# Performance work log

Measured on AMD Instinct MI355X. Metric: run time of the kernel, lower is better.

## Reference

```python
import jax, jax.numpy as jnp
import numpy as np

BLOCKS = 8
SSM_SIZE = 512
D_MODEL = 1024
DT_MIN = 1e-3
DT_MAX = 0.1
STEP_RESCALE = 1.0
BATCH = 4
SEQ_LEN = 4096


def _make_dplr_hippo(N):
    # numpy double-precision HiPPO-LegS -> DPLR init (done once at setup)
    n = np.arange(N, dtype=np.float64)
    P = np.sqrt(1.0 + 2.0 * n)
    A = -(np.tril(P[:, None] * P[None, :]) - np.diag(n))
    Pv = np.sqrt(n + 0.5)
    S = A + Pv[:, None] * Pv[None, :]
    Lambda_real = np.mean(np.diag(S)) + np.ones(N)
    Lambda_imag, V = np.linalg.eigh(S * -1j)  # V: (N, N) complex
    return Lambda_real + 1j * Lambda_imag, V


def _block_diag(M, reps):
    N = M.shape[0]
    out = np.zeros((N * reps, N * reps), dtype=M.dtype)
    for i in range(reps):
        out[i * N:(i + 1) * N, i * N:(i + 1) * N] = M
    return out


def setup_inputs() -> dict:
    key = jax.random.key(0)
    k1, k2, k3, k4, k5 = jax.random.split(key, 5)
    bs = SSM_SIZE // BLOCKS
    Lam_blk, V_blk = _make_dplr_hippo(bs)
    Lambda = np.tile(Lam_blk, BLOCKS)                     # (ssm_size,)
    V = _block_diag(V_blk, BLOCKS)                        # (ssm_size, ssm_size)
    Vinv = _block_diag(V_blk.conj().T, BLOCKS)

    Vc = jnp.asarray(V, dtype=jnp.complex64)
    Vinvc = jnp.asarray(Vinv, dtype=jnp.complex64)

    B0 = jax.random.normal(k1, (SSM_SIZE, D_MODEL), dtype=jnp.float32)
    VinvB = Vinvc @ B0.astype(jnp.complex64)              # (ssm_size, d_model)
    B = jnp.stack([VinvB.real, VinvB.imag], axis=-1)      # (ssm_size, d_model, 2)

    C0 = jax.random.normal(k2, (D_MODEL, SSM_SIZE, 2), dtype=jnp.float32)
    CV = (C0[..., 0] + 1j * C0[..., 1]).astype(jnp.complex64) @ Vc
    C = jnp.stack([CV.real, CV.imag], axis=-1)            # (d_model, ssm_size, 2)

    D = jax.random.normal(k3, (D_MODEL,), dtype=jnp.float32)
    step = jnp.log(jax.random.uniform(k4, (SSM_SIZE, 1)) * (DT_MAX - DT_MIN) + DT_MIN)

    u = jax.random.normal(k5, (BATCH, SEQ_LEN, D_MODEL), dtype=jnp.float32)
    return {
        "u": u,
        "Lambda_re": jnp.asarray(Lambda.real, dtype=jnp.float32),
        "Lambda_imag": jnp.asarray(Lambda.imag, dtype=jnp.float32),
        "B": B,
        "C": C,
        "D": D,
        "step": step,
    }


def _scan_binop(e1, e2):
    a1, b1 = e1
    a2, b2 = e2
    return a1 * a2, a2 * b1 + b2


def reference(u, Lambda_re, Lambda_imag, B, C, D, step):
    # clip_eigs=True
    Lambda = jnp.minimum(Lambda_re, -1e-4) + 1j * Lambda_imag      # (N,) complex
    B_tilde = B[..., 0] + 1j * B[..., 1]                           # (N, H)
    C_tilde = C[..., 0] + 1j * C[..., 1]                           # (H, N)
    dt = STEP_RESCALE * jnp.exp(step.squeeze(-1))                  # (N,)
    # ZOH discretization
    Lambda_bar = jnp.exp(Lambda * dt)                              # (N,)
    B_bar = ((Lambda_bar - 1.0) / Lambda)[:, None] * B_tilde       # (N, H)
    # input projection into state space
    Bu = u.astype(jnp.complex64) @ B_bar.T                         # (B, L, N)
    # linear recurrence x_t = Lambda_bar * x_{t-1} + Bu_t via associative scan
    A = jnp.broadcast_to(Lambda_bar, Bu.shape)
    _, state = jax.lax.associative_scan(_scan_binop, (A, Bu), axis=1)  # (B, L, N)
    y = (state @ C_tilde.T).real + D * u                           # (B, L, H)
    y = jax.nn.relu(y)
    return y, state
```

## Files before the change

### kernel.cpp

```cpp
#include <hip/hip_runtime.h>
#include <hip/hip_bf16.h>

typedef __attribute__((ext_vector_type(8))) short short8;
typedef __attribute__((ext_vector_type(4))) float f32x4;

#define DEVI __device__ __forceinline__

constexpr int SEQ = 4096;
constexpr int HD = 1024;
constexpr int NS = 512;
constexpr int NB = 4;
constexpr int MROWS = NB * SEQ;
constexpr int NCH = 64;
constexpr int CLEN = SEQ / NCH;

constexpr size_t MB = 1024 * 1024;
constexpr size_t OFF_UBF = 0;
constexpr size_t OFF_W1  = 32 * MB;
constexpr size_t OFF_W2  = 34 * MB;
constexpr size_t OFF_P   = 36 * MB;
constexpr size_t OFF_BU  = 36 * MB + 65536;
constexpr size_t OFF_T   = OFF_BU + 32 * MB;
constexpr size_t OFF_CRY = OFF_T + 1 * MB;
constexpr size_t OFF_SBF = OFF_CRY + 1 * MB;
constexpr size_t OFF_STF = OFF_SBF + 32 * MB;

DEVI float bf2f(unsigned short u) {
    union { unsigned u32; float f; } x; x.u32 = (unsigned)u << 16; return x.f;
}

__global__ void prep_params(const float* __restrict__ Lre, const float* __restrict__ Lim,
                            const float* __restrict__ step, float* __restrict__ P) {
    int n = blockIdx.x * 64 + threadIdx.x;
    if (n >= NS) return;
    float dt  = expf(step[n]);
    float lre = fminf(Lre[n], -1e-4f);
    float lim = Lim[n];
    float wre = lre * dt, wim = lim * dt;
    float s, c;
    sincosf(wim, &s, &c);
    float e = expf(wre);
    float lbre = e * c, lbim = e * s;
    float em1 = expm1f(wre);
    float sh  = sinf(0.5f * wim);
    float nr  = em1 * c - 2.0f * sh * sh;
    float ni  = e * s;
    float d2  = lre * lre + lim * lim;
    float inv = 1.0f / d2;
    float fre = (nr * lre + ni * lim) * inv;
    float fim = (ni * lre - nr * lim) * inv;
    float* p = P + n * 6;
    p[0] = wre; p[1] = wim; p[2] = lbre; p[3] = lbim; p[4] = fre; p[5] = fim;
}

__global__ void build_weights(const float* __restrict__ Bin, const float* __restrict__ Cin,
                              const float* __restrict__ P,
                              __hip_bfloat16* __restrict__ W1t,
                              __hip_bfloat16* __restrict__ W2t) {
    int bid = blockIdx.x;
    if (bid < 2048) {
        int idx = bid * 256 + threadIdx.x;
        int n = idx >> 10, k = idx & 1023;
        float fre = P[n * 6 + 4], fim = P[n * 6 + 5];
        float bre = Bin[(size_t)idx * 2 + 0], bim = Bin[(size_t)idx * 2 + 1];
        W1t[(size_t)(2 * n) * HD + k]     = __float2bfloat16(fre * bre - fim * bim);
        W1t[(size_t)(2 * n + 1) * HD + k] = __float2bfloat16(fre * bim + fim * bre);
    } else {
        int idx = (bid - 2048) * 256 + threadIdx.x;
        int h = idx >> 9, n = idx & 511;
        float cre = Cin[(size_t)idx * 2 + 0], cim = Cin[(size_t)idx * 2 + 1];
        W2t[(size_t)h * HD + 2 * n]     = __float2bfloat16(cre);
        W2t[(size_t)h * HD + 2 * n + 1] = __float2bfloat16(-cim);
    }
}

__global__ void cast_to_bf16(const float* __restrict__ x, __hip_bfloat16* __restrict__ y, int n8) {
    int i = blockIdx.x * 256 + threadIdx.x;
    if (i >= n8) return;
    const float4* xv = (const float4*)x;
    float4 a = xv[2 * (size_t)i], b = xv[2 * (size_t)i + 1];
    union { __hip_bfloat16 h[8]; short8 v; } u8;
    u8.h[0] = __float2bfloat16(a.x); u8.h[1] = __float2bfloat16(a.y);
    u8.h[2] = __float2bfloat16(a.z); u8.h[3] = __float2bfloat16(a.w);
    u8.h[4] = __float2bfloat16(b.x); u8.h[5] = __float2bfloat16(b.y);
    u8.h[6] = __float2bfloat16(b.z); u8.h[7] = __float2bfloat16(b.w);
    *((short8*)(y + (size_t)i * 8)) = u8.v;
}

DEVI void gload16(const __hip_bfloat16* g, __hip_bfloat16* l) {
    __builtin_amdgcn_global_load_lds(
        (const __attribute__((address_space(1))) unsigned int*)g,
        (__attribute__((address_space(3))) unsigned int*)l,
        16, 0, 0);
}

#define BARRIER_RAW() { asm volatile("" ::: "memory"); __builtin_amdgcn_s_barrier(); asm volatile("" ::: "memory"); }

template <int EPI>
__global__ __launch_bounds__(512, 2) void gemm_bf16_256(
    const __hip_bfloat16* __restrict__ A,
    const __hip_bfloat16* __restrict__ Bt,
    void* __restrict__ CoutV,
    const float* __restrict__ Dvec,
    const __hip_bfloat16* __restrict__ Ubf)
{
    __shared__ __hip_bfloat16 As[2][256 * 64];
    __shared__ __hip_bfloat16 Bs[2][256 * 64];
    const int tid  = threadIdx.x;
    const int lane = tid & 63;
    const int wid  = tid >> 6;
    const size_t bm = (size_t)blockIdx.x * 256;
    const size_t bn = (size_t)blockIdx.y * 256;
    const int wr = (wid >> 2) * 128;
    const int wc = (wid & 3) * 64;
    const int fr = lane & 15;
    const int fq = lane >> 4;

    f32x4 acc[8][4];
#pragma unroll
    for (int i = 0; i < 8; ++i)
#pragma unroll
        for (int j = 0; j < 4; ++j) acc[i][j] = (f32x4){0.f, 0.f, 0.f, 0.f};

    const int srow = tid >> 3;
    const int schk = tid & 7;

#define STAGE(buf, kt)                                                          \
    {                                                                           \
        _Pragma("unroll")                                                       \
        for (int q = 0; q < 4; ++q) {                                           \
            int row = q * 64 + srow;                                            \
            int gcol = (schk ^ (row & 7)) * 8;                                  \
            gload16(A  + (bm + row) * 1024 + (kt) + gcol, &As[buf][(row * 8 + schk) * 8]); \
            gload16(Bt + (bn + row) * 1024 + (kt) + gcol, &Bs[buf][(row * 8 + schk) * 8]); \
        }                                                                       \
    }

    STAGE(0, 0);
    __syncthreads();

    int cur = 0;
    for (int t = 0; t < 16; ++t) {
        if (t < 15) {
            STAGE(cur ^ 1, (t + 1) * 64);
            asm volatile("s_waitcnt vmcnt(8)" ::: "memory");
        } else {
            asm volatile("s_waitcnt vmcnt(0)" ::: "memory");
        }
        __builtin_amdgcn_sched_barrier(0);
        BARRIER_RAW();

#pragma unroll
        for (int kh = 0; kh < 2; ++kh) {
            short8 af[8], bf_[4];
#pragma unroll
            for (int m = 0; m < 8; ++m) {
                int r = wr + m * 16 + fr;
                int pc = (kh * 4 + fq) ^ (r & 7);
                af[m] = *(const short8*)(&As[cur][(r * 8 + pc) * 8]);
            }
#pragma unroll
            for (int n = 0; n < 4; ++n) {
                int r = wc + n * 16 + fr;
                int pc = (kh * 4 + fq) ^ (r & 7);
                bf_[n] = *(const short8*)(&Bs[cur][(r * 8 + pc) * 8]);
            }
#pragma unroll
            for (int m = 0; m < 8; ++m)
#pragma unroll
                for (int n = 0; n < 4; ++n)
                    acc[m][n] = __builtin_amdgcn_mfma_f32_16x16x32_bf16(af[m], bf_[n], acc[m][n], 0, 0, 0);
        }
        BARRIER_RAW();
        cur ^= 1;
    }
#undef STAGE

#pragma unroll
    for (int m = 0; m < 8; ++m)
#pragma unroll
        for (int n = 0; n < 4; ++n) {
            size_t col = bn + wc + n * 16 + fr;
            float dcol = (EPI == 1) ? Dvec[col] : 0.0f;
#pragma unroll
            for (int r = 0; r < 4; ++r) {
                size_t row = bm + wr + m * 16 + fq * 4 + r;
                float v = acc[m][n][r];
                if (EPI == 1) {
                    v = fmaf(dcol, __bfloat162float(Ubf[row * 1024 + col]), v);
                    ((float*)CoutV)[row * 1024 + col] = fmaxf(v, 0.0f);
                } else {
                    ((__hip_bfloat16*)CoutV)[row * 1024 + col] = __float2bfloat16(v);
                }
            }
        }
}

__global__ __launch_bounds__(256) void scan_totals(const unsigned* __restrict__ Bub,
                                                   const float* __restrict__ P,
                                                   float* __restrict__ T) {
    const int b = blockIdx.x >> 6;
    const int c = blockIdx.x & 63;
    const int t = threadIdx.x;
    const float l0r = P[t * 6 + 2], l0i = P[t * 6 + 3];
    const float l1r = P[(t + 256) * 6 + 2], l1i = P[(t + 256) * 6 + 3];
    const unsigned* base = Bub + ((size_t)(b * SEQ + c * CLEN)) * 512;
    float x0r = 0.f, x0i = 0.f, x1r = 0.f, x1i = 0.f;
    for (int j = 0; j < CLEN; ++j) {
        unsigned p0 = base[(size_t)j * 512 + t];
        unsigned p1 = base[(size_t)j * 512 + t + 256];
        float v0x = bf2f((unsigned short)(p0 & 0xffff)), v0y = bf2f((unsigned short)(p0 >> 16));
        float v1x = bf2f((unsigned short)(p1 & 0xffff)), v1y = bf2f((unsigned short)(p1 >> 16));
        float nr = fmaf(l0r, x0r, fmaf(-l0i, x0i, v0x));
        float ni = fmaf(l0r, x0i, fmaf(l0i, x0r, v0y));
        x0r = nr; x0i = ni;
        nr = fmaf(l1r, x1r, fmaf(-l1i, x1i, v1x));
        ni = fmaf(l1r, x1i, fmaf(l1i, x1r, v1y));
        x1r = nr; x1i = ni;
    }
    float2* Tp = (float2*)T;
    size_t o = ((size_t)(b * NCH + c)) * 512;
    Tp[o + t]       = make_float2(x0r, x0i);
    Tp[o + t + 256] = make_float2(x1r, x1i);
}

__global__ __launch_bounds__(256) void scan_carry(const float* __restrict__ T,
                                                  const float* __restrict__ P,
                                                  float* __restrict__ Cry) {
    int idx = blockIdx.x * 256 + threadIdx.x;
    if (idx >= NB * NS) return;
    int b = idx >> 9, n = idx & 511;
    float wre = P[n * 6 + 0] * (float)CLEN, wim = P[n * 6 + 1] * (float)CLEN;
    float s, c;
    sincosf(wim, &s, &c);
    float e = expf(wre);
    float cr = e * c, ci = e * s;
    float xr = 0.f, xi = 0.f;
    const float2* Tp = (const float2*)T;
    float2* Cp = (float2*)Cry;
    for (int ch = 0; ch < NCH; ++ch) {
        size_t o = ((size_t)(b * NCH + ch)) * 512 + n;
        Cp[o] = make_float2(xr, xi);
        float2 tv = Tp[o];
        float nr = fmaf(cr, xr, fmaf(-ci, xi, tv.x));
        float ni = fmaf(cr, xi, fmaf(ci, xr, tv.y));
        xr = nr; xi = ni;
    }
}

__global__ __launch_bounds__(256) void scan_final(const unsigned* __restrict__ Bub,
                                                  const float* __restrict__ P,
                                                  const float* __restrict__ Cry,
                                                  float* __restrict__ Sre,
                                                  __hip_bfloat16* __restrict__ Sbf) {
    const int b = blockIdx.x >> 6;
    const int c = blockIdx.x & 63;
    const int t = threadIdx.x;
    const float l0r = P[t * 6 + 2], l0i = P[t * 6 + 3];
    const float l1r = P[(t + 256) * 6 + 2], l1i = P[(t + 256) * 6 + 3];
    const unsigned* base = Bub + ((size_t)(b * SEQ + c * CLEN)) * 512;
    const float2* Cp = (const float2*)Cry;
    size_t co = ((size_t)(b * NCH + c)) * 512;
    float2 c0 = Cp[co + t], c1 = Cp[co + t + 256];
    float x0r = c0.x, x0i = c0.y, x1r = c1.x, x1i = c1.y;
    for (int j = 0; j < CLEN; ++j) {
        unsigned p0 = base[(size_t)j * 512 + t];
        unsigned p1 = base[(size_t)j * 512 + t + 256];
        float v0x = bf2f((unsigned short)(p0 & 0xffff)), v0y = bf2f((unsigned short)(p0 >> 16));
        float v1x = bf2f((unsigned short)(p1 & 0xffff)), v1y = bf2f((unsigned short)(p1 >> 16));
        float nr = fmaf(l0r, x0r, fmaf(-l0i, x0i, v0x));
        float ni = fmaf(l0r, x0i, fmaf(l0i, x0r, v0y));
        x0r = nr; x0i = ni;
        nr = fmaf(l1r, x1r, fmaf(-l1i, x1i, v1x));
        ni = fmaf(l1r, x1i, fmaf(l1i, x1r, v1y));
        x1r = nr; x1i = ni;
        size_t m = (size_t)b * SEQ + c * CLEN + j;
        Sre[m * 512 + t]       = x0r;
        Sre[m * 512 + t + 256] = x1r;
        union { __hip_bfloat16 h[2]; unsigned uu; } q0, q1;
        q0.h[0] = __float2bfloat16(x0r); q0.h[1] = __float2bfloat16(x0i);
        q1.h[0] = __float2bfloat16(x1r); q1.h[1] = __float2bfloat16(x1i);
        *((unsigned*)(Sbf + m * 1024 + 2 * t))       = q0.uu;
        *((unsigned*)(Sbf + m * 1024 + 2 * t + 512)) = q1.uu;
    }
}

extern "C" void kernel_launch(void* const* d_in, const int* in_sizes, int n_in,
                              void* d_out, int out_size, void* d_ws, size_t ws_size,
                              hipStream_t stream) {
    const float* u    = (const float*)d_in[0];
    const float* Lre  = (const float*)d_in[1];
    const float* Lim  = (const float*)d_in[2];
    const float* Bin  = (const float*)d_in[3];
    const float* Cin  = (const float*)d_in[4];
    const float* Dv   = (const float*)d_in[5];
    const float* step = (const float*)d_in[6];

    char* ws = (char*)d_ws;
    __hip_bfloat16* Ubf = (__hip_bfloat16*)(ws + OFF_UBF);
    __hip_bfloat16* W1t = (__hip_bfloat16*)(ws + OFF_W1);
    __hip_bfloat16* W2t = (__hip_bfloat16*)(ws + OFF_W2);
    float*          P   = (float*)(ws + OFF_P);
    __hip_bfloat16* Bu  = (__hip_bfloat16*)(ws + OFF_BU);
    float*          T   = (float*)(ws + OFF_T);
    float*          Cry = (float*)(ws + OFF_CRY);
    __hip_bfloat16* Sbf = (__hip_bfloat16*)(ws + OFF_SBF);

    float* y_out = (float*)d_out;
    constexpr int Y_ELEMS = MROWS * HD;
    constexpr int S_ELEMS = MROWS * NS;
    float* state_out = (out_size >= Y_ELEMS + S_ELEMS) ? (y_out + Y_ELEMS)
                                                       : (float*)(ws + OFF_STF);

    prep_params<<<8, 64, 0, stream>>>(Lre, Lim, step, P);
    build_weights<<<4096, 256, 0, stream>>>(Bin, Cin, P, W1t, W2t);
    cast_to_bf16<<<(MROWS * HD / 8) / 256, 256, 0, stream>>>(u, Ubf, MROWS * HD / 8);

    dim3 gg(MROWS / 256, HD / 256);
    gemm_bf16_256<0><<<gg, 512, 0, stream>>>(Ubf, W1t, (void*)Bu, nullptr, nullptr);

    scan_totals<<<NB * NCH, 256, 0, stream>>>((const unsigned*)Bu, P, T);
    scan_carry<<<(NB * NS + 255) / 256, 256, 0, stream>>>(T, P, Cry);
    scan_final<<<NB * NCH, 256, 0, stream>>>((const unsigned*)Bu, P, Cry, state_out, Sbf);

    gemm_bf16_256<1><<<gg, 512, 0, stream>>>(Sbf, W2t, (void*)y_out, Dv, Ubf);
}
```

Baseline: 138.1 us.

## Double scan chunk count, vectorize scan accesses, raise MFMA wave priority

Doubles the number of sequence chunks in the chunked scan, from 64 to 128, so the totals and final scan passes launch twice as many blocks, each with a shorter serial loop. The carry pass becomes longer, and the totals and carry buffers grow to fit. Each scan thread now handles two adjacent states, so loads and stores become 8- and 16-byte vector accesses instead of two strided 4-byte ones. The GEMM inner loop also raises wave priority around its MFMA block with s_setprio.

After: 145.7 us. 1.06x slower.

```diff
diff --git a/kernel.cpp b/kernel.cpp
--- a/kernel.cpp
+++ b/kernel.cpp
@@ -11,7 +11,7 @@
 constexpr int NS = 512;
 constexpr int NB = 4;
 constexpr int MROWS = NB * SEQ;
-constexpr int NCH = 64;
+constexpr int NCH = 128;
 constexpr int CLEN = SEQ / NCH;
 
 constexpr size_t MB = 1024 * 1024;
@@ -21,8 +21,8 @@
 constexpr size_t OFF_P   = 36 * MB;
 constexpr size_t OFF_BU  = 36 * MB + 65536;
 constexpr size_t OFF_T   = OFF_BU + 32 * MB;
-constexpr size_t OFF_CRY = OFF_T + 1 * MB;
-constexpr size_t OFF_SBF = OFF_CRY + 1 * MB;
+constexpr size_t OFF_CRY = OFF_T + 2 * MB;
+constexpr size_t OFF_SBF = OFF_CRY + 2 * MB;
 constexpr size_t OFF_STF = OFF_SBF + 32 * MB;
 
 DEVI float bf2f(unsigned short u) {
@@ -165,11 +165,13 @@
                 int pc = (kh * 4 + fq) ^ (r & 7);
                 bf_[n] = *(const short8*)(&Bs[cur][(r * 8 + pc) * 8]);
             }
+            __builtin_amdgcn_s_setprio(1);
 #pragma unroll
             for (int m = 0; m < 8; ++m)
 #pragma unroll
                 for (int n = 0; n < 4; ++n)
                     acc[m][n] = __builtin_amdgcn_mfma_f32_16x16x32_bf16(af[m], bf_[n], acc[m][n], 0, 0, 0);
+            __builtin_amdgcn_s_setprio(0);
         }
         BARRIER_RAW();
         cur ^= 1;
@@ -199,18 +201,18 @@
 __global__ __launch_bounds__(256) void scan_totals(const unsigned* __restrict__ Bub,
                                                    const float* __restrict__ P,
                                                    float* __restrict__ T) {
-    const int b = blockIdx.x >> 6;
-    const int c = blockIdx.x & 63;
+    const int b = blockIdx.x >> 7;
+    const int c = blockIdx.x & 127;
     const int t = threadIdx.x;
-    const float l0r = P[t * 6 + 2], l0i = P[t * 6 + 3];
-    const float l1r = P[(t + 256) * 6 + 2], l1i = P[(t + 256) * 6 + 3];
-    const unsigned* base = Bub + ((size_t)(b * SEQ + c * CLEN)) * 512;
+    const int n0 = 2 * t, n1 = 2 * t + 1;
+    const float l0r = P[n0 * 6 + 2], l0i = P[n0 * 6 + 3];
+    const float l1r = P[n1 * 6 + 2], l1i = P[n1 * 6 + 3];
+    const uint2* base = (const uint2*)(Bub + ((size_t)(b * SEQ + c * CLEN)) * 512);
     float x0r = 0.f, x0i = 0.f, x1r = 0.f, x1i = 0.f;
     for (int j = 0; j < CLEN; ++j) {
-        unsigned p0 = base[(size_t)j * 512 + t];
-        unsigned p1 = base[(size_t)j * 512 + t + 256];
-        float v0x = bf2f((unsigned short)(p0 & 0xffff)), v0y = bf2f((unsigned short)(p0 >> 16));
-        float v1x = bf2f((unsigned short)(p1 & 0xffff)), v1y = bf2f((unsigned short)(p1 >> 16));
+        uint2 p = base[(size_t)j * 256 + t];
+        float v0x = bf2f((unsigned short)(p.x & 0xffff)), v0y = bf2f((unsigned short)(p.x >> 16));
+        float v1x = bf2f((unsigned short)(p.y & 0xffff)), v1y = bf2f((unsigned short)(p.y >> 16));
         float nr = fmaf(l0r, x0r, fmaf(-l0i, x0i, v0x));
         float ni = fmaf(l0r, x0i, fmaf(l0i, x0r, v0y));
         x0r = nr; x0i = ni;
@@ -218,10 +220,8 @@
         ni = fmaf(l1r, x1i, fmaf(l1i, x1r, v1y));
         x1r = nr; x1i = ni;
     }
-    float2* Tp = (float2*)T;
-    size_t o = ((size_t)(b * NCH + c)) * 512;
-    Tp[o + t]       = make_float2(x0r, x0i);
-    Tp[o + t + 256] = make_float2(x1r, x1i);
+    float4* Tp = (float4*)(T + ((size_t)(b * NCH + c)) * 1024);
+    Tp[t] = make_float4(x0r, x0i, x1r, x1i);
 }
 
 __global__ __launch_bounds__(256) void scan_carry(const float* __restrict__ T,
@@ -253,21 +253,20 @@
                                                   const float* __restrict__ Cry,
                                                   float* __restrict__ Sre,
                                                   __hip_bfloat16* __restrict__ Sbf) {
-    const int b = blockIdx.x >> 6;
-    const int c = blockIdx.x & 63;
+    const int b = blockIdx.x >> 7;
+    const int c = blockIdx.x & 127;
     const int t = threadIdx.x;
-    const float l0r = P[t * 6 + 2], l0i = P[t * 6 + 3];
-    const float l1r = P[(t + 256) * 6 + 2], l1i = P[(t + 256) * 6 + 3];
-    const unsigned* base = Bub + ((size_t)(b * SEQ + c * CLEN)) * 512;
-    const float2* Cp = (const float2*)Cry;
-    size_t co = ((size_t)(b * NCH + c)) * 512;
-    float2 c0 = Cp[co + t], c1 = Cp[co + t + 256];
-    float x0r = c0.x, x0i = c0.y, x1r = c1.x, x1i = c1.y;
+    const int n0 = 2 * t, n1 = 2 * t + 1;
+    const float l0r = P[n0 * 6 + 2], l0i = P[n0 * 6 + 3];
+    const float l1r = P[n1 * 6 + 2], l1i = P[n1 * 6 + 3];
+    const uint2* base = (const uint2*)(Bub + ((size_t)(b * SEQ + c * CLEN)) * 512);
+    const float4* Cp = (const float4*)(Cry + ((size_t)(b * NCH + c)) * 1024);
+    float4 c01 = Cp[t];
+    float x0r = c01.x, x0i = c01.y, x1r = c01.z, x1i = c01.w;
     for (int j = 0; j < CLEN; ++j) {
-        unsigned p0 = base[(size_t)j * 512 + t];
-        unsigned p1 = base[(size_t)j * 512 + t + 256];
-        float v0x = bf2f((unsigned short)(p0 & 0xffff)), v0y = bf2f((unsigned short)(p0 >> 16));
-        float v1x = bf2f((unsigned short)(p1 & 0xffff)), v1y = bf2f((unsigned short)(p1 >> 16));
+        uint2 p = base[(size_t)j * 256 + t];
+        float v0x = bf2f((unsigned short)(p.x & 0xffff)), v0y = bf2f((unsigned short)(p.x >> 16));
+        float v1x = bf2f((unsigned short)(p.y & 0xffff)), v1y = bf2f((unsigned short)(p.y >> 16));
         float nr = fmaf(l0r, x0r, fmaf(-l0i, x0i, v0x));
         float ni = fmaf(l0r, x0i, fmaf(l0i, x0r, v0y));
         x0r = nr; x0i = ni;
@@ -275,13 +274,11 @@
         ni = fmaf(l1r, x1i, fmaf(l1i, x1r, v1y));
         x1r = nr; x1i = ni;
         size_t m = (size_t)b * SEQ + c * CLEN + j;
-        Sre[m * 512 + t]       = x0r;
-        Sre[m * 512 + t + 256] = x1r;
+        ((float2*)(Sre + m * 512))[t] = make_float2(x0r, x1r);
         union { __hip_bfloat16 h[2]; unsigned uu; } q0, q1;
         q0.h[0] = __float2bfloat16(x0r); q0.h[1] = __float2bfloat16(x0i);
         q1.h[0] = __float2bfloat16(x1r); q1.h[1] = __float2bfloat16(x1i);
-        *((unsigned*)(Sbf + m * 1024 + 2 * t))       = q0.uu;
-        *((unsigned*)(Sbf + m * 1024 + 2 * t + 512)) = q1.uu;
+        ((uint2*)(Sbf + m * 1024))[t] = make_uint2(q0.uu, q1.uu);
     }
 }
 
```
